# Performance work log

Hardware: AMD Instinct MI355X
Metric: run time of the kernel (lower is better)

## Reference

```python
import jax, jax.numpy as jnp
import numpy as np

GAMMA = 0.01   # module default gamma
STEP = 10      # forward subsamples time axis with x[::10]
BIG = 1e10     # finite stand-in for +inf boundary (exp(-BIG/gamma) underflows to 0 exactly)


def _softdtw(D, gamma):
    """Batched soft-DTW DP over cost matrices D: (B, N, M) -> (B,).
    Anti-diagonal wavefront: lax.scan over the 2*max(N,M)-1 diagonals,
    each diagonal updated fully vectorized (mirrors compute_softdtw_cuda).
    """
    B, N, M = D.shape
    inv_g = 1.0 / gamma
    # padded R, boundaries at BIG (acts as +inf), R[:,0,0] = 0
    R0 = jnp.full((B, N + 2, M + 2), BIG, dtype=D.dtype).at[:, 0, 0].set(0.0)
    ii = jnp.arange(1, N + 1)  # padded row indices on a diagonal

    def step(R, p):
        jj = p + 2 - ii                      # i + j = p + 2 in padded coords
        valid = (jj >= 1) & (jj <= M)
        jc = jnp.clip(jj, 1, M)
        r0 = -R[:, ii - 1, jc - 1] * inv_g   # diag neighbor
        r1 = -R[:, ii - 1, jc] * inv_g       # up neighbor
        r2 = -R[:, ii, jc - 1] * inv_g       # left neighbor
        rmax = jnp.maximum(jnp.maximum(r0, r1), r2)
        rsum = jnp.exp(r0 - rmax) + jnp.exp(r1 - rmax) + jnp.exp(r2 - rmax)
        softmin = -gamma * (jnp.log(rsum) + rmax)
        new = D[:, ii - 1, jc - 1] + softmin
        R = R.at[:, ii, jc].set(jnp.where(valid[None, :], new, R[:, ii, jc]))
        return R, None

    R, _ = jax.lax.scan(step, R0, jnp.arange(N + M - 1))
    return R[:, N, M]


def _loss(x, y):
    # x, y: (nt, nr, nc). Subsample time by STEP; treat each (r, c) trace as a
    # batch-1, dim-1 sequence; sum soft-DTW values over all nr*nc traces.
    xs = x[::STEP]                      # (L, nr, nc)
    ys = y[::STEP]
    L = xs.shape[0]
    X = xs.reshape(L, -1).T             # (B, L), B = nr*nc
    Y = ys.reshape(L, -1).T
    D = (X[:, :, None] - Y[:, None, :]) ** 2  # squared-Euclidean cost, d=1
    return jnp.sum(_softdtw(D, GAMMA)).reshape(1)


def setup_inputs() -> dict:
    key = jax.random.key(0)
    k1, k2 = jax.random.split(key)
    x = jax.random.normal(k1, (2048, 128, 2), dtype=jnp.float32)
    y = jax.random.normal(k2, (2048, 128, 2), dtype=jnp.float32)
    return {"x": x, "y": y}


def reference(x, y):
    return _loss(x, y)
```

## Files before the change

kernel.cpp:

```cpp
#include <hip/hip_runtime.h>

#define STEP 10
#define NCH  256
#define CSCL (-144.2695041f)
#define GLN2 (-0.00693147181f)
#define BIGP (-1.442695041e12f)
#define YOFF 64
#define YLDS 384
#define BNDSZ 472
#define NW   4

__device__ __forceinline__ float fexp2(float x){ float r; asm("v_exp_f32 %0, %1" : "=v"(r) : "v"(x)); return r; }
__device__ __forceinline__ float flog2(float x){ float r; asm("v_log_f32 %0, %1" : "=v"(r) : "v"(x)); return r; }

__device__ __forceinline__ float dpp_shr1(float src){
    int s = __builtin_bit_cast(int, src);
    int r = __builtin_amdgcn_update_dpp(0, s, 0x138 , 0xF, 0xF, true);
    return __builtin_bit_cast(float, r);
}

__device__ __forceinline__ float dpcell(float up2, float up, float left, float qq) {
    float m  = fmaxf(fmaxf(up2, up), left);
    float lo = fminf(fminf(up2, up), left);
    float md = __builtin_amdgcn_fmed3f(up2, up, left);
    float e  = fexp2(lo - m) + fexp2(md - m) + 1.0f;
    float mq = m + qq;
    return flog2(e) + mq;
}

__global__ __launch_bounds__(256, 1)
void softdtw_wave(const float* __restrict__ x, const float* __restrict__ y,
                  float* __restrict__ ws, int N) {
    const int b = blockIdx.x;
    const int t = threadIdx.x;
    const int l = t & 63;
    const int w = t >> 6;

    __shared__ __align__(16) float Ys[YLDS];
    __shared__ float bnd[NW - 1][BNDSZ];
    __shared__ int prog[NW - 1];

    for (int j = t; j < YLDS; j += 256) Ys[j] = 0.f;
    float* bf = &bnd[0][0];
    for (int j = t; j < (NW - 1) * BNDSZ; j += 256) bf[j] = BIGP;
    if (t < NW - 1) prog[t] = 0;
    __syncthreads();
    for (int j = t; j < N; j += 256) Ys[YOFF + j] = y[j * STEP * NCH + b];
    __syncthreads();

    const int i = 64 * w + l + 1;
    const float xv = (i <= N) ? x[(i - 1) * STEP * NCH + b] : 0.f;

    float sp = BIGP, bp = BIGP;
    float bq = (t == 0) ? 0.0f : BIGP;

    const int smax = 2 * N;
    const int sb0  = 64 * w + 2;
    const int myrows = (64 * (w + 1) < N) ? 64 * (w + 1) : N;
    const int NG     = (myrows + N - sb0 + 1 + 7) >> 3;
    const bool prod = (w < NW - 1);
    const bool cons = (w > 0);
    const int prows = (64 * w < N) ? 64 * w : N;
    const int pNG   = (prows + N - (sb0 - 64) + 1 + 7) >> 3;
    const int progFinal = (sb0 - 64) + 8 * pNG - 1;

    const float* yb = Ys + (YOFF - l);
    const float* bb = cons ? bnd[w - 1] : bnd[0];

    #define POLL(NEED) do {                                               \
        const int need_ = min((NEED), progFinal);                         \
        while (__hip_atomic_load(&prog[w - 1], __ATOMIC_ACQUIRE,          \
                                 __HIP_MEMORY_SCOPE_WORKGROUP) < need_)   \
            __builtin_amdgcn_s_sleep(1);                                  \
    } while (0)

    float q0,q1,q2,q3,q4,q5,q6,q7;
    float h0,h1,h2,h3,h4,h5,h6,h7;
    {
        float a0=yb[0],a1=yb[1],a2=yb[2],a3=yb[3];
        float a4=yb[4],a5=yb[5],a6=yb[6],a7=yb[7];
        if (cons) {
            POLL(sb0 + 7);
            if (l == 0) bp = bb[sb0 - 1];
            h0=bb[sb0+0]; h1=bb[sb0+1]; h2=bb[sb0+2]; h3=bb[sb0+3];
            h4=bb[sb0+4]; h5=bb[sb0+5]; h6=bb[sb0+6]; h7=bb[sb0+7];
        } else {
            h0=h1=h2=h3=h4=h5=h6=h7 = BIGP;
        }
        float d;
        d=xv-a0; q0=d*CSCL*d;  d=xv-a1; q1=d*CSCL*d;
        d=xv-a2; q2=d*CSCL*d;  d=xv-a3; q3=d*CSCL*d;
        d=xv-a4; q4=d*CSCL*d;  d=xv-a5; q5=d*CSCL*d;
        d=xv-a6; q6=d*CSCL*d;  d=xv-a7; q7=d*CSCL*d;
    }

    #define STEPJ(QQ, HJ, CJ, J) do {                              \
        CJ = dpcell(bq, bp, sp, (QQ));                             \
        float sh = dpp_shr1(CJ);                                   \
        bq = bp;                                                   \
        bp = (l == 0) ? (HJ) : sh;                                 \
        sp = CJ;                                                   \
        if (sb + (J) == smax && i == N) ws[b] = CJ * GLN2;         \
    } while (0)

    for (int m = 0; m < NG; ++m) {
        const int sb = sb0 + 8 * m;
        float c0,c1,c2,c3,c4,c5,c6,c7;
        STEPJ(q0, h0, c0, 0); STEPJ(q1, h1, c1, 1);
        STEPJ(q2, h2, c2, 2); STEPJ(q3, h3, c3, 3);
        STEPJ(q4, h4, c4, 4); STEPJ(q5, h5, c5, 5);
        STEPJ(q6, h6, c6, 6); STEPJ(q7, h7, c7, 7);

        if (prod && l == 63) {
            float* bw = &bnd[w][sb];
            bw[0]=c0; bw[1]=c1; bw[2]=c2; bw[3]=c3;
            bw[4]=c4; bw[5]=c5; bw[6]=c6; bw[7]=c7;
            __hip_atomic_store(&prog[w], sb + 7, __ATOMIC_RELEASE,
                               __HIP_MEMORY_SCOPE_WORKGROUP);
        }

        if (m + 1 < NG) {
            const float* yn = yb + 8 * (m + 1);
            float a0=yn[0],a1=yn[1],a2=yn[2],a3=yn[3];
            float a4=yn[4],a5=yn[5],a6=yn[6],a7=yn[7];
            if (cons) {
                POLL(sb + 15);
                h0=bb[sb+8];  h1=bb[sb+9];  h2=bb[sb+10]; h3=bb[sb+11];
                h4=bb[sb+12]; h5=bb[sb+13]; h6=bb[sb+14]; h7=bb[sb+15];
            }
            float d;
            d=xv-a0; q0=d*CSCL*d;  d=xv-a1; q1=d*CSCL*d;
            d=xv-a2; q2=d*CSCL*d;  d=xv-a3; q3=d*CSCL*d;
            d=xv-a4; q4=d*CSCL*d;  d=xv-a5; q5=d*CSCL*d;
            d=xv-a6; q6=d*CSCL*d;  d=xv-a7; q7=d*CSCL*d;
        }
    }
    #undef STEPJ
    #undef POLL
}

__global__ __launch_bounds__(256)
void reduce256(const float* __restrict__ ws, float* __restrict__ out) {
    const int tid = threadIdx.x;
    float v = ws[tid];
    #pragma unroll
    for (int off = 32; off > 0; off >>= 1)
        v += __shfl_down(v, off, 64);
    __shared__ float partial[4];
    if ((tid & 63) == 0) partial[tid >> 6] = v;
    __syncthreads();
    if (tid == 0) out[0] = (partial[0] + partial[1]) + (partial[2] + partial[3]);
}

extern "C" void kernel_launch(void* const* d_in, const int* in_sizes, int n_in,
                              void* d_out, int out_size, void* d_ws, size_t ws_size,
                              hipStream_t stream) {
    const float* x = (const float*)d_in[0];
    const float* y = (const float*)d_in[1];
    float* out = (float*)d_out;
    float* ws  = (float*)d_ws;

    const int T = in_sizes[0] / NCH;
    const int L = (T + STEP - 1) / STEP;

    softdtw_wave<<<dim3(NCH), dim3(256), 0, stream>>>(x, y, ws, L);
    reduce256<<<dim3(1), dim3(256), 0, stream>>>(ws, out);
}
```

Baseline: 38.17 us.

## Represent soft-DTW cells as mantissa-exponent pairs to drop per-cell exp/log

Replaces the log-domain soft-min recurrence (max/min/med3, two exp2 and one log2 per cell) with a linear-domain recurrence that stores each cell as a float mantissa plus an integer exponent. Neighbours are aligned with ldexp and summed, and the cost term becomes a precomputed exp2 factor. The carried cell is renormalised once per 8-step group, and boundary values now travel as separate mantissa and exponent arrays. The critical dependency chain trades transcendentals for integer max, ldexp and a multiply, at the cost of more instructions per cell, twice the LDS boundary traffic, and possible mantissa drift or accuracy loss.

```diff
diff --git a/kernel.cpp b/kernel.cpp
--- a/kernel.cpp
+++ b/kernel.cpp
@@ -4,28 +4,24 @@
 #define NCH  256
 #define CSCL (-144.2695041f)
 #define GLN2 (-0.00693147181f)
-#define BIGP (-1.442695041e12f)
 #define YOFF 64
 #define YLDS 384
-#define BNDSZ 472
+#define BNDSZ 424
 #define NW   4
+#define EWALL (-(1 << 27))
 
 __device__ __forceinline__ float fexp2(float x){ float r; asm("v_exp_f32 %0, %1" : "=v"(r) : "v"(x)); return r; }
 __device__ __forceinline__ float flog2(float x){ float r; asm("v_log_f32 %0, %1" : "=v"(r) : "v"(x)); return r; }
+__device__ __forceinline__ float fldexp(float x, int e){ float r; asm("v_ldexp_f32 %0, %1, %2" : "=v"(r) : "v"(x), "v"(e)); return r; }
+__device__ __forceinline__ float fmant(float x){ float r; asm("v_frexp_mant_f32 %0, %1" : "=v"(r) : "v"(x)); return r; }
+__device__ __forceinline__ int   fexpi(float x){ int r; asm("v_frexp_exp_i32_f32 %0, %1" : "=v"(r) : "v"(x)); return r; }
 
-__device__ __forceinline__ float dpp_shr1(float src){
-    int s = __builtin_bit_cast(int, src);
-    int r = __builtin_amdgcn_update_dpp(0, s, 0x138 , 0xF, 0xF, true);
-    return __builtin_bit_cast(float, r);
+__device__ __forceinline__ float dppf(float h, float s){
+    int o = __builtin_bit_cast(int, h), xx = __builtin_bit_cast(int, s);
+    return __builtin_bit_cast(float, __builtin_amdgcn_update_dpp(o, xx, 0x138, 0xF, 0xF, false));
 }
-
-__device__ __forceinline__ float dpcell(float up2, float up, float left, float qq) {
-    float m  = fmaxf(fmaxf(up2, up), left);
-    float lo = fminf(fminf(up2, up), left);
-    float md = __builtin_amdgcn_fmed3f(up2, up, left);
-    float e  = fexp2(lo - m) + fexp2(md - m) + 1.0f;
-    float mq = m + qq;
-    return flog2(e) + mq;
+__device__ __forceinline__ int dppi(int h, int s){
+    return __builtin_amdgcn_update_dpp(h, s, 0x138, 0xF, 0xF, false);
 }
 
 __global__ __launch_bounds__(256, 1)
@@ -37,12 +33,13 @@
     const int w = t >> 6;
 
     __shared__ __align__(16) float Ys[YLDS];
-    __shared__ float bnd[NW - 1][BNDSZ];
+    __shared__ float bndM[NW - 1][BNDSZ];
+    __shared__ int   bndE[NW - 1][BNDSZ];
     __shared__ int prog[NW - 1];
 
     for (int j = t; j < YLDS; j += 256) Ys[j] = 0.f;
-    float* bf = &bnd[0][0];
-    for (int j = t; j < (NW - 1) * BNDSZ; j += 256) bf[j] = BIGP;
+    float* bfM = &bndM[0][0]; int* bfE = &bndE[0][0];
+    for (int j = t; j < (NW - 1) * BNDSZ; j += 256) { bfM[j] = 0.f; bfE[j] = EWALL; }
     if (t < NW - 1) prog[t] = 0;
     __syncthreads();
     for (int j = t; j < N; j += 256) Ys[YOFF + j] = y[j * STEP * NCH + b];
@@ -51,8 +48,8 @@
     const int i = 64 * w + l + 1;
     const float xv = (i <= N) ? x[(i - 1) * STEP * NCH + b] : 0.f;
 
-    float sp = BIGP, bp = BIGP;
-    float bq = (t == 0) ? 0.0f : BIGP;
+    float msp = 0.f, mbp = 0.f, mbq = (t == 0) ? 1.0f : 0.f;
+    int   esp = EWALL, ebp = EWALL, ebq = (t == 0) ? 0 : EWALL;
 
     const int smax = 2 * N;
     const int sb0  = 64 * w + 2;
@@ -64,8 +61,9 @@
     const int pNG   = (prows + N - (sb0 - 64) + 1 + 7) >> 3;
     const int progFinal = (sb0 - 64) + 8 * pNG - 1;
 
-    const float* yb = Ys + (YOFF - l);
-    const float* bb = cons ? bnd[w - 1] : bnd[0];
+    const float* yrow = Ys + (YOFF - l);
+    const float* bbM = cons ? bndM[w - 1] : bndM[0];
+    const int*   bbE = cons ? bndE[w - 1] : bndE[0];
 
     #define POLL(NEED) do {                                               \
         const int need_ = min((NEED), progFinal);                         \
@@ -74,68 +72,87 @@
             __builtin_amdgcn_s_sleep(1);                                  \
     } while (0)
 
-    float q0,q1,q2,q3,q4,q5,q6,q7;
-    float h0,h1,h2,h3,h4,h5,h6,h7;
+    #define QPREP(AY, MQ, EQ) do {                      \
+        float d_ = xv - (AY);                           \
+        float q_ = d_ * CSCL * d_;                      \
+        float f_ = floorf(q_);                          \
+        (EQ) = (int)f_;                                 \
+        (MQ) = fexp2(q_ - f_);                          \
+    } while (0)
+
+    float mq0,mq1,mq2,mq3,mq4,mq5,mq6,mq7;  int eq0,eq1,eq2,eq3,eq4,eq5,eq6,eq7;
+    float hm0,hm1,hm2,hm3,hm4,hm5,hm6,hm7;  int he0,he1,he2,he3,he4,he5,he6,he7;
+
     {
-        float a0=yb[0],a1=yb[1],a2=yb[2],a3=yb[3];
-        float a4=yb[4],a5=yb[5],a6=yb[6],a7=yb[7];
+        float a0=yrow[0],a1=yrow[1],a2=yrow[2],a3=yrow[3];
+        float a4=yrow[4],a5=yrow[5],a6=yrow[6],a7=yrow[7];
         if (cons) {
             POLL(sb0 + 7);
-            if (l == 0) bp = bb[sb0 - 1];
-            h0=bb[sb0+0]; h1=bb[sb0+1]; h2=bb[sb0+2]; h3=bb[sb0+3];
-            h4=bb[sb0+4]; h5=bb[sb0+5]; h6=bb[sb0+6]; h7=bb[sb0+7];
+            if (l == 0) { mbp = bbM[sb0 - 1]; ebp = bbE[sb0 - 1]; }
+            hm0=bbM[sb0+0]; hm1=bbM[sb0+1]; hm2=bbM[sb0+2]; hm3=bbM[sb0+3];
+            hm4=bbM[sb0+4]; hm5=bbM[sb0+5]; hm6=bbM[sb0+6]; hm7=bbM[sb0+7];
+            he0=bbE[sb0+0]; he1=bbE[sb0+1]; he2=bbE[sb0+2]; he3=bbE[sb0+3];
+            he4=bbE[sb0+4]; he5=bbE[sb0+5]; he6=bbE[sb0+6]; he7=bbE[sb0+7];
         } else {
-            h0=h1=h2=h3=h4=h5=h6=h7 = BIGP;
+            hm0=hm1=hm2=hm3=hm4=hm5=hm6=hm7 = 0.f;
+            he0=he1=he2=he3=he4=he5=he6=he7 = EWALL;
         }
-        float d;
-        d=xv-a0; q0=d*CSCL*d;  d=xv-a1; q1=d*CSCL*d;
-        d=xv-a2; q2=d*CSCL*d;  d=xv-a3; q3=d*CSCL*d;
-        d=xv-a4; q4=d*CSCL*d;  d=xv-a5; q5=d*CSCL*d;
-        d=xv-a6; q6=d*CSCL*d;  d=xv-a7; q7=d*CSCL*d;
+        QPREP(a0,mq0,eq0); QPREP(a1,mq1,eq1); QPREP(a2,mq2,eq2); QPREP(a3,mq3,eq3);
+        QPREP(a4,mq4,eq4); QPREP(a5,mq5,eq5); QPREP(a6,mq6,eq6); QPREP(a7,mq7,eq7);
     }
 
-    #define STEPJ(QQ, HJ, CJ, J) do {                              \
-        CJ = dpcell(bq, bp, sp, (QQ));                             \
-        float sh = dpp_shr1(CJ);                                   \
-        bq = bp;                                                   \
-        bp = (l == 0) ? (HJ) : sh;                                 \
-        sp = CJ;                                                   \
-        if (sb + (J) == smax && i == N) ws[b] = CJ * GLN2;         \
+    #define STEPJ(MQ, EQ, HM, HE, CM, CE, J) do {                        \
+        int e1_ = ebq > ebp ? ebq : ebp; e1_ = e1_ > esp ? e1_ : esp;    \
+        float a_ = fldexp(mbq, ebq - e1_);                               \
+        float b_ = fldexp(mbp, ebp - e1_);                               \
+        float c_ = fldexp(msp, esp - e1_);                               \
+        CM = ((a_ + b_) + c_) * (MQ);                                    \
+        CE = e1_ + (EQ);                                                 \
+        float nm_ = dppf((HM), CM);                                      \
+        int   ne_ = dppi((HE), CE);                                      \
+        mbq = mbp; ebq = ebp; mbp = nm_; ebp = ne_;                      \
+        msp = CM;  esp = CE;                                             \
+        if (sb + (J) == smax && i == N)                                  \
+            ws[b] = GLN2 * ((float)CE + flog2(CM));                      \
     } while (0)
 
     for (int m = 0; m < NG; ++m) {
         const int sb = sb0 + 8 * m;
-        float c0,c1,c2,c3,c4,c5,c6,c7;
-        STEPJ(q0, h0, c0, 0); STEPJ(q1, h1, c1, 1);
-        STEPJ(q2, h2, c2, 2); STEPJ(q3, h3, c3, 3);
-        STEPJ(q4, h4, c4, 4); STEPJ(q5, h5, c5, 5);
-        STEPJ(q6, h6, c6, 6); STEPJ(q7, h7, c7, 7);
+        float c0,c1,c2,c3,c4,c5,c6,c7;  int g0,g1,g2,g3,g4,g5,g6,g7;
+        STEPJ(mq0,eq0,hm0,he0,c0,g0,0); STEPJ(mq1,eq1,hm1,he1,c1,g1,1);
+        STEPJ(mq2,eq2,hm2,he2,c2,g2,2); STEPJ(mq3,eq3,hm3,he3,c3,g3,3);
+        STEPJ(mq4,eq4,hm4,he4,c4,g4,4); STEPJ(mq5,eq5,hm5,he5,c5,g5,5);
+        STEPJ(mq6,eq6,hm6,he6,c6,g6,6); STEPJ(mq7,eq7,hm7,he7,c7,g7,7);
 
         if (prod && l == 63) {
-            float* bw = &bnd[w][sb];
-            bw[0]=c0; bw[1]=c1; bw[2]=c2; bw[3]=c3;
-            bw[4]=c4; bw[5]=c5; bw[6]=c6; bw[7]=c7;
+            float* bwM = &bndM[w][sb];  int* bwE = &bndE[w][sb];
+            bwM[0]=c0; bwM[1]=c1; bwM[2]=c2; bwM[3]=c3;
+            bwM[4]=c4; bwM[5]=c5; bwM[6]=c6; bwM[7]=c7;
+            bwE[0]=g0; bwE[1]=g1; bwE[2]=g2; bwE[3]=g3;
+            bwE[4]=g4; bwE[5]=g5; bwE[6]=g6; bwE[7]=g7;
             __hip_atomic_store(&prog[w], sb + 7, __ATOMIC_RELEASE,
                                __HIP_MEMORY_SCOPE_WORKGROUP);
         }
 
+        { int kr = fexpi(msp); msp = fmant(msp); esp += kr; }
+
         if (m + 1 < NG) {
-            const float* yn = yb + 8 * (m + 1);
+            const float* yn = yrow + 8 * (m + 1);
             float a0=yn[0],a1=yn[1],a2=yn[2],a3=yn[3];
             float a4=yn[4],a5=yn[5],a6=yn[6],a7=yn[7];
             if (cons) {
                 POLL(sb + 15);
-                h0=bb[sb+8];  h1=bb[sb+9];  h2=bb[sb+10]; h3=bb[sb+11];
-                h4=bb[sb+12]; h5=bb[sb+13]; h6=bb[sb+14]; h7=bb[sb+15];
+                hm0=bbM[sb+8];  hm1=bbM[sb+9];  hm2=bbM[sb+10]; hm3=bbM[sb+11];
+                hm4=bbM[sb+12]; hm5=bbM[sb+13]; hm6=bbM[sb+14]; hm7=bbM[sb+15];
+                he0=bbE[sb+8];  he1=bbE[sb+9];  he2=bbE[sb+10]; he3=bbE[sb+11];
+                he4=bbE[sb+12]; he5=bbE[sb+13]; he6=bbE[sb+14]; he7=bbE[sb+15];
             }
-            float d;
-            d=xv-a0; q0=d*CSCL*d;  d=xv-a1; q1=d*CSCL*d;
-            d=xv-a2; q2=d*CSCL*d;  d=xv-a3; q3=d*CSCL*d;
-            d=xv-a4; q4=d*CSCL*d;  d=xv-a5; q5=d*CSCL*d;
-            d=xv-a6; q6=d*CSCL*d;  d=xv-a7; q7=d*CSCL*d;
+            QPREP(a0,mq0,eq0); QPREP(a1,mq1,eq1); QPREP(a2,mq2,eq2); QPREP(a3,mq3,eq3);
+            QPREP(a4,mq4,eq4); QPREP(a5,mq5,eq5); QPREP(a6,mq6,eq6); QPREP(a7,mq7,eq7);
         }
     }
     #undef STEPJ
+    #undef QPREP
     #undef POLL
 }
 
```

New measurement: 46.38 us. +21.5%, slower.

## Fuse final reduction into wavefront kernel via last-block atomic counter

Applied to the files above, without the earlier changes.

Removes the separate reduce kernel launch: each block publishes its result, increments a global counter, and the last block to finish does the 256-way sum. A memset of the counter is added to the stream. The DPP boundary select is folded into the DPP instruction's old-value operand, and the cell's add order is rearranged. The boundary buffer size is also trimmed. The risks are the extra memset launch and the need for correct atomic ordering between blocks.

```diff
diff --git a/kernel.cpp b/kernel.cpp
--- a/kernel.cpp
+++ b/kernel.cpp
@@ -7,15 +7,16 @@
 #define BIGP (-1.442695041e12f)
 #define YOFF 64
 #define YLDS 384
-#define BNDSZ 472
+#define BNDSZ 424
 #define NW   4
 
 __device__ __forceinline__ float fexp2(float x){ float r; asm("v_exp_f32 %0, %1" : "=v"(r) : "v"(x)); return r; }
 __device__ __forceinline__ float flog2(float x){ float r; asm("v_log_f32 %0, %1" : "=v"(r) : "v"(x)); return r; }
 
-__device__ __forceinline__ float dpp_shr1(float src){
+__device__ __forceinline__ float dpp_shr1_sel(float h, float src){
+    int o = __builtin_bit_cast(int, h);
     int s = __builtin_bit_cast(int, src);
-    int r = __builtin_amdgcn_update_dpp(0, s, 0x138 , 0xF, 0xF, true);
+    int r = __builtin_amdgcn_update_dpp(o, s, 0x138 , 0xF, 0xF, false);
     return __builtin_bit_cast(float, r);
 }
 
@@ -24,13 +25,14 @@
     float lo = fminf(fminf(up2, up), left);
     float md = __builtin_amdgcn_fmed3f(up2, up, left);
     float e  = fexp2(lo - m) + fexp2(md - m) + 1.0f;
-    float mq = m + qq;
-    return flog2(e) + mq;
+    float ls = flog2(e) + m;
+    return ls + qq;
 }
 
 __global__ __launch_bounds__(256, 1)
 void softdtw_wave(const float* __restrict__ x, const float* __restrict__ y,
-                  float* __restrict__ ws, int N) {
+                  float* __restrict__ ws, int* __restrict__ cnt,
+                  float* __restrict__ out, int N) {
     const int b = blockIdx.x;
     const int t = threadIdx.x;
     const int l = t & 63;
@@ -39,6 +41,8 @@
     __shared__ __align__(16) float Ys[YLDS];
     __shared__ float bnd[NW - 1][BNDSZ];
     __shared__ int prog[NW - 1];
+    __shared__ float res_s;
+    __shared__ int last_s;
 
     for (int j = t; j < YLDS; j += 256) Ys[j] = 0.f;
     float* bf = &bnd[0][0];
@@ -64,7 +68,7 @@
     const int pNG   = (prows + N - (sb0 - 64) + 1 + 7) >> 3;
     const int progFinal = (sb0 - 64) + 8 * pNG - 1;
 
-    const float* yb = Ys + (YOFF - l);
+    const float* yrow = Ys + (YOFF - l);
     const float* bb = cons ? bnd[w - 1] : bnd[0];
 
     #define POLL(NEED) do {                                               \
@@ -77,8 +81,8 @@
     float q0,q1,q2,q3,q4,q5,q6,q7;
     float h0,h1,h2,h3,h4,h5,h6,h7;
     {
-        float a0=yb[0],a1=yb[1],a2=yb[2],a3=yb[3];
-        float a4=yb[4],a5=yb[5],a6=yb[6],a7=yb[7];
+        float a0=yrow[0],a1=yrow[1],a2=yrow[2],a3=yrow[3];
+        float a4=yrow[4],a5=yrow[5],a6=yrow[6],a7=yrow[7];
         if (cons) {
             POLL(sb0 + 7);
             if (l == 0) bp = bb[sb0 - 1];
@@ -96,11 +100,9 @@
 
     #define STEPJ(QQ, HJ, CJ, J) do {                              \
         CJ = dpcell(bq, bp, sp, (QQ));                             \
-        float sh = dpp_shr1(CJ);                                   \
-        bq = bp;                                                   \
-        bp = (l == 0) ? (HJ) : sh;                                 \
-        sp = CJ;                                                   \
-        if (sb + (J) == smax && i == N) ws[b] = CJ * GLN2;         \
+        float n_ = dpp_shr1_sel((HJ), CJ);                         \
+        bq = bp; bp = n_; sp = CJ;                                 \
+        if (sb + (J) == smax && i == N) res_s = CJ * GLN2;         \
     } while (0)
 
     for (int m = 0; m < NG; ++m) {
@@ -120,7 +122,7 @@
         }
 
         if (m + 1 < NG) {
-            const float* yn = yb + 8 * (m + 1);
+            const float* yn = yrow + 8 * (m + 1);
             float a0=yn[0],a1=yn[1],a2=yn[2],a3=yn[3];
             float a4=yn[4],a5=yn[5],a6=yn[6],a7=yn[7];
             if (cons) {
@@ -137,19 +139,27 @@
     }
     #undef STEPJ
     #undef POLL
-}
 
-__global__ __launch_bounds__(256)
-void reduce256(const float* __restrict__ ws, float* __restrict__ out) {
-    const int tid = threadIdx.x;
-    float v = ws[tid];
-    #pragma unroll
-    for (int off = 32; off > 0; off >>= 1)
-        v += __shfl_down(v, off, 64);
-    __shared__ float partial[4];
-    if ((tid & 63) == 0) partial[tid >> 6] = v;
     __syncthreads();
-    if (tid == 0) out[0] = (partial[0] + partial[1]) + (partial[2] + partial[3]);
+    if (t == 0) {
+        __hip_atomic_store(&ws[b], res_s, __ATOMIC_RELEASE,
+                           __HIP_MEMORY_SCOPE_AGENT);
+        int prev = __hip_atomic_fetch_add(cnt, 1, __ATOMIC_ACQ_REL,
+                                          __HIP_MEMORY_SCOPE_AGENT);
+        last_s = (prev == NCH - 1);
+    }
+    __syncthreads();
+    if (last_s) {
+        float v = __hip_atomic_load(&ws[t], __ATOMIC_RELAXED,
+                                    __HIP_MEMORY_SCOPE_AGENT);
+        #pragma unroll
+        for (int off = 32; off > 0; off >>= 1)
+            v += __shfl_down(v, off, 64);
+        __shared__ float partial[4];
+        if ((t & 63) == 0) partial[t >> 6] = v;
+        __syncthreads();
+        if (t == 0) out[0] = (partial[0] + partial[1]) + (partial[2] + partial[3]);
+    }
 }
 
 extern "C" void kernel_launch(void* const* d_in, const int* in_sizes, int n_in,
@@ -159,10 +169,11 @@
     const float* y = (const float*)d_in[1];
     float* out = (float*)d_out;
     float* ws  = (float*)d_ws;
+    int*   cnt = (int*)(ws + NCH);
 
     const int T = in_sizes[0] / NCH;
     const int L = (T + STEP - 1) / STEP;
 
-    softdtw_wave<<<dim3(NCH), dim3(256), 0, stream>>>(x, y, ws, L);
-    reduce256<<<dim3(1), dim3(256), 0, stream>>>(ws, out);
+    hipMemsetAsync(cnt, 0, sizeof(int), stream);
+    softdtw_wave<<<dim3(NCH), dim3(256), 0, stream>>>(x, y, ws, cnt, out, L);
 }
```

After: 48.44 us. 1.27x slower.
